# Kernel optimization log

Hardware: AMD Instinct MI355X
Metric: run time of the kernel (lower is better)

## Reference

```python
import jax, jax.numpy as jnp
import numpy as np

B, N, MAX_ITER = 8, 192, 3


def setup_inputs() -> dict:
    key = jax.random.key(0)
    k1, k2 = jax.random.split(key)
    s_span = jax.random.normal(k1, (B, N, N), jnp.float32)
    s_pair = jax.random.normal(k2, (B, N, N, N), jnp.float32)
    # valid constituent spans: strictly upper-triangular (i < j), full-length sentences
    mask = jnp.broadcast_to(jnp.triu(jnp.ones((N, N), bool), 1)[None], (B, N, N))
    return {"s_span": s_span, "s_pair": s_pair, "mask": mask}


def _mfvi(s_span, s_pair, mask, max_iter=MAX_ITER):
    # s_span: [B,N,N], s_pair: [B,N,N,N] (b,i,j,k), mask: [B,N,N] bool
    n = mask.shape[-1]
    idx = jnp.arange(n)
    ls = jnp.minimum(idx[:, None], idx[None, :])  # min(i,j), [N,N]
    rs = jnp.maximum(idx[:, None], idx[None, :])  # max(i,j), [N,N]
    # mask2o[b,i,j,k] = mask[b,i,j] & (min(i,j) != k) & (max(i,j) != k)
    valid_k = (ls[:, :, None] != idx) & (rs[:, :, None] != idx)  # [N,N,N]
    mask2o = mask[:, :, :, None] & valid_k[None]                 # [B,N,N,N]
    sp = s_pair * mask2o.astype(s_pair.dtype)
    q = s_span
    for _ in range(max_iter):
        # q_new[b,i,j] = s_span[b,i,j] + sum_k sigmoid(q)[b,i,k] * sp[b,i,j,k]
        q = s_span + jnp.einsum('bik,bijk->bij', jax.nn.sigmoid(q), sp)
    return q


def reference(s_span, s_pair, mask):
    logits = _mfvi(s_span, s_pair, mask)
    return jax.nn.sigmoid(logits)  # marginals [B,N,N]
```

## Files before the change

### kernel.cpp

```cpp
#include <hip/hip_runtime.h>


#define NDIM 192
#define TPB 768
#define ROUNDS 12
#define RSTRIDE 52

__device__ __forceinline__ float sigmoidf(float x) {
    return 1.0f / (1.0f + __expf(-x));
}

__global__ __launch_bounds__(TPB, 6)
void mfvi_fused_kernel(const float* __restrict__ s_span,
                       const float* __restrict__ s_pair,
                       float* __restrict__ out)
{
    const int row = blockIdx.x;
    const int i   = row % NDIM;
    const int t   = threadIdx.x;
    const int g   = t / 48;
    const int m   = t % 48;
    const int kb  = m * 4;

    __shared__ __align__(16) float ssp[NDIM];
    __shared__ __align__(16) float v[NDIM];
    __shared__ __align__(16) float red[NDIM * RSTRIDE];

    const float4* sp4 = (const float4*)(s_pair + (size_t)row * (NDIM * NDIM));
    float4 R[ROUNDS];
#pragma unroll
    for (int r = 0; r < ROUNDS; ++r)
        R[r] = sp4[r * TPB + t];

    if (t < NDIM) {
        float s = s_span[(size_t)row * NDIM + t];
        ssp[t] = s;
        v[t]   = sigmoidf(s);
    }

#pragma unroll
    for (int r = 0; r < ROUNDS; ++r) {
        const int j  = r * 16 + g;
        const bool rv = (i < j);
        float4 q = R[r];
        q.x = (rv && (kb + 0) != i && (kb + 0) != j) ? q.x : 0.0f;
        q.y = (rv && (kb + 1) != i && (kb + 1) != j) ? q.y : 0.0f;
        q.z = (rv && (kb + 2) != i && (kb + 2) != j) ? q.z : 0.0f;
        q.w = (rv && (kb + 3) != i && (kb + 3) != j) ? q.w : 0.0f;
        R[r] = q;
    }

    __syncthreads();

    float sig = 0.0f;
#pragma unroll 1
    for (int iter = 0; iter < 3; ++iter) {
        const float4 vv = ((const float4*)v)[m];
#pragma unroll
        for (int r = 0; r < ROUNDS; ++r) {
            const int j = r * 16 + g;
            red[j * RSTRIDE + m] = R[r].x * vv.x + R[r].y * vv.y
                                 + R[r].z * vv.z + R[r].w * vv.w;
        }
        __syncthreads();

        if (t < NDIM) {
            const float4* rr = (const float4*)(&red[t * RSTRIDE]);
            float sum = 0.0f;
#pragma unroll
            for (int u = 0; u < 12; ++u) {
                float4 a = rr[u];
                sum += (a.x + a.y) + (a.z + a.w);
            }
            sig  = sigmoidf(ssp[t] + sum);
            v[t] = sig;
        }
        __syncthreads();
    }

    if (t < NDIM)
        out[(size_t)row * NDIM + t] = sig;
}

extern "C" void kernel_launch(void* const* d_in, const int* in_sizes, int n_in,
                              void* d_out, int out_size, void* d_ws, size_t ws_size,
                              hipStream_t stream) {
    const float* s_span = (const float*)d_in[0];
    const float* s_pair = (const float*)d_in[1];
    float* out = (float*)d_out;

    const int rows = 8 * NDIM;
    mfvi_fused_kernel<<<rows, TPB, 0, stream>>>(s_span, s_pair, out);
}
```

Baseline: 310.5 us.

## Make kernel persistent over six rows with register double-buffered prefetch

```diff
diff --git a/kernel.cpp b/kernel.cpp
--- a/kernel.cpp
+++ b/kernel.cpp
@@ -2,84 +2,111 @@
 
 
 #define NDIM 192
-#define TPB 768
-#define ROUNDS 12
+#define TPB  768
+#define F4PT 12
 #define RSTRIDE 52
+#define ROWS_PER_BLK 6
+#define NBLK 256
 
 __device__ __forceinline__ float sigmoidf(float x) {
     return 1.0f / (1.0f + __expf(-x));
 }
 
-__global__ __launch_bounds__(TPB, 6)
-void mfvi_fused_kernel(const float* __restrict__ s_span,
-                       const float* __restrict__ s_pair,
-                       float* __restrict__ out)
+__device__ __forceinline__ void lds_barrier() {
+    asm volatile("s_waitcnt lgkmcnt(0)\n\ts_barrier" ::: "memory");
+}
+
+__global__ __launch_bounds__(TPB, 3)
+void mfvi_persistent(const float* __restrict__ s_span,
+                     const float* __restrict__ s_pair,
+                     float* __restrict__ out)
 {
-    const int row = blockIdx.x;
-    const int i   = row % NDIM;
+    const int blk = blockIdx.x;
     const int t   = threadIdx.x;
     const int g   = t / 48;
     const int m   = t % 48;
     const int kb  = m * 4;
 
-    __shared__ __align__(16) float ssp[NDIM];
     __shared__ __align__(16) float v[NDIM];
     __shared__ __align__(16) float red[NDIM * RSTRIDE];
 
-    const float4* sp4 = (const float4*)(s_pair + (size_t)row * (NDIM * NDIM));
-    float4 R[ROUNDS];
+    float4 R[2][F4PT];
+    float  sspn[2];
+
+    {
+        const int row0 = blk * ROWS_PER_BLK;
+        const float4* sp4 = (const float4*)(s_pair + (size_t)row0 * (NDIM * NDIM));
 #pragma unroll
-    for (int r = 0; r < ROUNDS; ++r)
-        R[r] = sp4[r * TPB + t];
-
-    if (t < NDIM) {
-        float s = s_span[(size_t)row * NDIM + t];
-        ssp[t] = s;
-        v[t]   = sigmoidf(s);
+        for (int r = 0; r < F4PT; ++r)
+            R[0][r] = sp4[r * TPB + t];
+        if (t < NDIM)
+            sspn[0] = s_span[(size_t)row0 * NDIM + t];
     }
 
 #pragma unroll
-    for (int r = 0; r < ROUNDS; ++r) {
-        const int j  = r * 16 + g;
-        const bool rv = (i < j);
-        float4 q = R[r];
-        q.x = (rv && (kb + 0) != i && (kb + 0) != j) ? q.x : 0.0f;
-        q.y = (rv && (kb + 1) != i && (kb + 1) != j) ? q.y : 0.0f;
-        q.z = (rv && (kb + 2) != i && (kb + 2) != j) ? q.z : 0.0f;
-        q.w = (rv && (kb + 3) != i && (kb + 3) != j) ? q.w : 0.0f;
-        R[r] = q;
+    for (int s = 0; s < ROWS_PER_BLK; ++s) {
+        const int cur = s & 1, nxt = cur ^ 1;
+        const int row = blk * ROWS_PER_BLK + s;
+        const int i   = row % NDIM;
+
+        if (s + 1 < ROWS_PER_BLK) {
+            const int row2 = row + 1;
+            const float4* sp4 = (const float4*)(s_pair + (size_t)row2 * (NDIM * NDIM));
+#pragma unroll
+            for (int r = 0; r < F4PT; ++r)
+                R[nxt][r] = sp4[r * TPB + t];
+            if (t < NDIM)
+                sspn[nxt] = s_span[(size_t)row2 * NDIM + t];
+        }
+
+#pragma unroll
+        for (int r = 0; r < F4PT; ++r) {
+            const int j  = r * 16 + g;
+            const bool rv = (i < j);
+            float4 q = R[cur][r];
+            q.x = (rv && (kb + 0) != i && (kb + 0) != j) ? q.x : 0.0f;
+            q.y = (rv && (kb + 1) != i && (kb + 1) != j) ? q.y : 0.0f;
+            q.z = (rv && (kb + 2) != i && (kb + 2) != j) ? q.z : 0.0f;
+            q.w = (rv && (kb + 3) != i && (kb + 3) != j) ? q.w : 0.0f;
+            R[cur][r] = q;
+        }
+
+        float myspan = 0.0f;
+        if (t < NDIM) {
+            myspan = sspn[cur];
+            v[t]   = sigmoidf(myspan);
+        }
+        lds_barrier();
+
+        float sig = 0.0f;
+#pragma unroll
+        for (int it = 0; it < 3; ++it) {
+            const float4 vv = ((const float4*)v)[m];
+#pragma unroll
+            for (int r = 0; r < F4PT; ++r) {
+                const int j = r * 16 + g;
+                red[j * RSTRIDE + m] = R[cur][r].x * vv.x + R[cur][r].y * vv.y
+                                     + R[cur][r].z * vv.z + R[cur][r].w * vv.w;
+            }
+            lds_barrier();
+
+            if (t < NDIM) {
+                const float4* rr = (const float4*)(&red[t * RSTRIDE]);
+                float sum = 0.0f;
+#pragma unroll
+                for (int u = 0; u < 12; ++u) {
+                    float4 a = rr[u];
+                    sum += (a.x + a.y) + (a.z + a.w);
+                }
+                sig  = sigmoidf(myspan + sum);
+                v[t] = sig;
+            }
+            lds_barrier();
+        }
+
+        if (t < NDIM)
+            out[(size_t)row * NDIM + t] = sig;
     }
-
-    __syncthreads();
-
-    float sig = 0.0f;
-#pragma unroll 1
-    for (int iter = 0; iter < 3; ++iter) {
-        const float4 vv = ((const float4*)v)[m];
-#pragma unroll
-        for (int r = 0; r < ROUNDS; ++r) {
-            const int j = r * 16 + g;
-            red[j * RSTRIDE + m] = R[r].x * vv.x + R[r].y * vv.y
-                                 + R[r].z * vv.z + R[r].w * vv.w;
-        }
-        __syncthreads();
-
-        if (t < NDIM) {
-            const float4* rr = (const float4*)(&red[t * RSTRIDE]);
-            float sum = 0.0f;
-#pragma unroll
-            for (int u = 0; u < 12; ++u) {
-                float4 a = rr[u];
-                sum += (a.x + a.y) + (a.z + a.w);
-            }
-            sig  = sigmoidf(ssp[t] + sum);
-            v[t] = sig;
-        }
-        __syncthreads();
-    }
-
-    if (t < NDIM)
-        out[(size_t)row * NDIM + t] = sig;
 }
 
 extern "C" void kernel_launch(void* const* d_in, const int* in_sizes, int n_in,
@@ -89,6 +116,5 @@
     const float* s_pair = (const float*)d_in[1];
     float* out = (float*)d_out;
 
-    const int rows = 8 * NDIM;
-    mfvi_fused_kernel<<<rows, TPB, 0, stream>>>(s_span, s_pair, out);
+    mfvi_persistent<<<NBLK, TPB, 0, stream>>>(s_span, s_pair, out);
 }
```

New measurement: 314.2 us. No clear change (+1.2%).
